# Optimization experiments

Hardware: AMD Instinct MI355X
Metric: run time of the kernel (lower is better)

Reference implementation:

```python
import jax, jax.numpy as jnp
import numpy as np
import math

N = 4096      # nodes
E = 131072    # edges (avg degree 32)
C = 128       # input channels
RATIO = 0.5   # TopKPooling default ratio
DIMS = [(128, 256), (256, 512), (512, 512), (512, 256), (256, 128)]


def setup_inputs() -> dict:
    key = jax.random.key(0)
    ks = jax.random.split(key, 16)
    inp = {}
    inp['x'] = jax.random.normal(ks[0], (N, C), jnp.float32)
    inp['edge_index'] = jax.random.randint(ks[1], (2, E), 0, N, jnp.int32)
    for i, (fi, fo) in enumerate(DIMS):
        inp[f'w{i}'] = jax.random.normal(ks[2 + i], (fi, fo), jnp.float32) / np.sqrt(fi).astype(np.float32)
        inp[f'b{i}'] = jnp.zeros((fo,), jnp.float32)
    inp['p0'] = jax.random.normal(ks[10], (256,), jnp.float32)
    inp['p1'] = jax.random.normal(ks[11], (512,), jnp.float32)
    return inp


def _gcn(x, M, w, b):
    # GCNConv: add self loops (weight 1), symmetric D^-1/2 normalization with
    # deg computed over target (col) index, aggregate messages src->dst.
    # M[r, c] = weight of edge (src=r, dst=c); dense equivalent of sparse conv.
    n = M.shape[0]
    Mc = M + jnp.eye(n, dtype=M.dtype)
    deg = Mc.sum(axis=0)
    dis = jnp.where(deg > 0, jax.lax.rsqrt(deg), 0.0)
    A = dis[:, None] * Mc * dis[None, :]          # normalized (src, dst)
    return jax.nn.relu(A.T @ (x @ w) + b)          # out[dst] = sum_src A * xW


def _augment(M):
    # augment_adj: add self loops then spspmm(A, A) -> dense (M+I) @ (M+I)
    B = M + jnp.eye(M.shape[0], dtype=M.dtype)
    return B @ B


def _pool(x, M, p):
    # TopKPooling: score = tanh(x.p / ||p||), keep top ceil(ratio*n) nodes,
    # gate kept features by score, slice adjacency to kept nodes.
    s = jnp.tanh((x @ p) / jnp.linalg.norm(p))
    k = int(math.ceil(RATIO * x.shape[0]))
    vals, perm = jax.lax.top_k(s, k)
    return x[perm] * vals[:, None], M[perm][:, perm], perm


def reference(x, edge_index, w0, b0, w1, b1, w2, b2, w3, b3, w4, b4, p0, p1):
    # dense adjacency M[src, dst] from edge list with unit edge weights
    M = jnp.zeros((N, N), jnp.float32).at[edge_index[0], edge_index[1]].add(1.0)

    # down block 0
    x = _gcn(x, M, w0, b0)
    res0, M0 = x, M
    x, M, perm0 = _pool(x, _augment(M), p0)

    # down block 1
    x = _gcn(x, M, w1, b1)
    res1, M1 = x, M
    x, M, perm1 = _pool(x, _augment(M), p1)

    # bottleneck
    x = _gcn(x, M, w2, b2)

    # up block 1: scatter into zeros, sum residual
    up = jnp.zeros_like(res1).at[perm1].set(x)
    x = _gcn(res1 + up, M1, w3, b3)

    # up block 0
    up = jnp.zeros_like(res0).at[perm0].set(x)
    x = _gcn(res0 + up, M0, w4, b4)
    return x
```

## Files before the change

kernel.cpp:

```cpp
#include <hip/hip_runtime.h>

#define NN 4096
#define EE 131072
#define NP1 2048
#define NP2 1024

typedef __attribute__((ext_vector_type(8))) __bf16 bf16x8;
typedef __attribute__((ext_vector_type(4))) float f32x4;
typedef __attribute__((ext_vector_type(8))) unsigned short ushort8;

static __device__ inline unsigned short bfbits(__bf16 b) {
  union { __bf16 x; unsigned short u; } c; c.x = b; return c.u;
}
static __device__ inline void split2(float v, unsigned short& h, unsigned short& l) {
  __bf16 hb = (__bf16)v;
  float hf = (float)hb;
  __bf16 lb = (__bf16)(v - hf);
  h = bfbits(hb); l = bfbits(lb);
}

static __device__ inline size_t pchunk(int r, int k, int NT) {
  return ((size_t)(r >> 4) * NT + (k >> 5)) * 64 + (((k >> 3) & 3) << 4) + (r & 15);
}


__global__ void hist_kernel(const int* __restrict__ src, const int* __restrict__ dst,
                            int* __restrict__ cnt_src, int* __restrict__ cnt_dst, int E) {
  int e = blockIdx.x * blockDim.x + threadIdx.x;
  if (e < E) {
    atomicAdd(&cnt_src[src[e]], 1);
    atomicAdd(&cnt_dst[dst[e]], 1);
  }
}

__global__ __launch_bounds__(1024) void scan2(const int* __restrict__ cnt_dst,
                                              const int* __restrict__ cnt_src,
                                              int* __restrict__ csc_off, int* __restrict__ csr_off,
                                              float* __restrict__ dis0, int n) {
  __shared__ int tmp[4096];
  const int* in = blockIdx.x ? cnt_src : cnt_dst;
  int* out = blockIdx.x ? csr_off : csc_off;
  int tid = threadIdx.x;
  for (int i = tid; i < n; i += 1024) {
    int v = in[i];
    tmp[i] = v;
    if (blockIdx.x == 0) dis0[i] = rsqrtf((float)v + 1.0f);
  }
  __syncthreads();
  for (int off = 1; off < n; off <<= 1) {
    int v[4];
    int c = 0;
    for (int i = tid; i < n; i += 1024) { v[c++] = (i >= off) ? tmp[i - off] : 0; }
    __syncthreads();
    c = 0;
    for (int i = tid; i < n; i += 1024) { tmp[i] += v[c++]; }
    __syncthreads();
  }
  for (int i = tid; i < n; i += 1024) out[i + 1] = tmp[i];
  if (tid == 0) out[0] = 0;
}

__global__ void scatter_kernel(const int* __restrict__ src, const int* __restrict__ dst,
                               const int* __restrict__ csc_off, const int* __restrict__ csr_off,
                               int* __restrict__ fill_dst, int* __restrict__ fill_src,
                               int* __restrict__ csc_src, int* __restrict__ csr_dst, int E) {
  int e = blockIdx.x * blockDim.x + threadIdx.x;
  if (e < E) {
    int s = src[e], d = dst[e];
    int p = atomicAdd(&fill_dst[d], 1);
    csc_src[csc_off[d] + p] = s;
    int q = atomicAdd(&fill_src[s], 1);
    csr_dst[csr_off[s] + q] = d;
  }
}

__global__ void pnorm2(const float* __restrict__ p0, const float* __restrict__ p1,
                       float* __restrict__ outv) {
  const float* p = blockIdx.x ? p1 : p0;
  int C = blockIdx.x ? 512 : 256;
  int tid = threadIdx.x;
  float acc = 0.f;
  for (int j = tid; j < C; j += 256) { float v = p[j]; acc += v * v; }
  for (int o = 32; o > 0; o >>= 1) acc += __shfl_down(acc, o);
  __shared__ float red[4];
  if ((tid & 63) == 0) red[tid >> 6] = acc;
  __syncthreads();
  if (tid == 0) outv[blockIdx.x] = sqrtf(red[0] + red[1] + red[2] + red[3]);
}


__global__ void score_key(const float* __restrict__ X, const float* __restrict__ p,
                          const float* __restrict__ pn, float* __restrict__ s,
                          unsigned long long* __restrict__ keys, int C) {
  int i = blockIdx.x;
  int tid = threadIdx.x;
  float acc = 0.f;
  for (int j = tid; j < C; j += 256) acc += X[(size_t)i * C + j] * p[j];
  for (int o = 32; o > 0; o >>= 1) acc += __shfl_down(acc, o);
  __shared__ float red[4];
  if ((tid & 63) == 0) red[tid >> 6] = acc;
  __syncthreads();
  if (tid == 0) {
    float sv = tanhf((red[0] + red[1] + red[2] + red[3]) / pn[0]);
    s[i] = sv;
    unsigned u = __float_as_uint(sv);
    unsigned m = (u & 0x80000000u) ? ~u : (u | 0x80000000u);
    keys[i] = (((unsigned long long)(~m)) << 32) | (unsigned)i;
  }
}

__global__ __launch_bounds__(256) void rank_count(const unsigned long long* __restrict__ keys,
                                                  int* __restrict__ rank) {
  __shared__ unsigned long long kk[512];
  int tid = threadIdx.x;
  int cand = blockIdx.x * 256 + tid;
  int base = blockIdx.y * 512;
  kk[tid] = keys[base + tid];
  kk[tid + 256] = keys[base + tid + 256];
  __syncthreads();
  unsigned long long kc = keys[cand];
  int c = 0;
#pragma unroll 8
  for (int t = 0; t < 512; ++t) c += (kk[t] < kc) ? 1 : 0;
  atomicAdd(&rank[cand], c);
}

__global__ void rank_place(const float* __restrict__ s, const int* __restrict__ rank, int k, int n,
                           int* __restrict__ kept, int* __restrict__ perm, float* __restrict__ vals,
                           int* __restrict__ cntk) {
  int i = blockIdx.x * blockDim.x + threadIdx.x;
  if (i < n) {
    int r = rank[i];
    int isk = (r < k) ? 1 : 0;
    if (isk) { perm[r] = i; vals[r] = s[i]; kept[i] = r; }
    else kept[i] = -1;
    if (cntk) cntk[i] = isk;
  }
}

__global__ void pool_split_p(const float* __restrict__ X, const int* __restrict__ perm,
                             const float* __restrict__ vals, unsigned short* __restrict__ h,
                             unsigned short* __restrict__ l, int C) {
  int a = blockIdx.x;
  int r = perm[a];
  float v = vals[a];
  int NT = C >> 5;
  for (int j0 = threadIdx.x * 8; j0 < C; j0 += 64 * 8) {
    ushort8 hv, lv;
#pragma unroll
    for (int e = 0; e < 8; ++e) {
      unsigned short he, le;
      split2(X[(size_t)r * C + j0 + e] * v, he, le);
      hv[e] = he; lv[e] = le;
    }
    size_t c = pchunk(a, j0, NT);
    *(ushort8*)&h[c * 8] = hv;
    *(ushort8*)&l[c * 8] = lv;
  }
}


__global__ __launch_bounds__(256) void aug_row_p(const int* __restrict__ csr_off,
                                                 const int* __restrict__ csr_dst,
                                                 const int* __restrict__ kept,
                                                 const int* __restrict__ perm,
                                                 unsigned short* __restrict__ rm) {
  __shared__ float acc[NP1];
  int ki = blockIdx.x;
  int r = perm[ki];
  for (int t = threadIdx.x; t < NP1; t += 256) acc[t] = 0.f;
  __syncthreads();
  int s = csr_off[r], e = csr_off[r + 1];
  int nm = e - s;
  int wave = threadIdx.x >> 6, lane = threadIdx.x & 63;
  for (int m = wave; m <= nm; m += 4) {
    int k = (m < nm) ? csr_dst[s + m] : r;
    int s2 = csr_off[k], e2 = csr_off[k + 1];
    int n2 = e2 - s2;
    for (int t = lane; t <= n2; t += 64) {
      int j = (t < n2) ? csr_dst[s2 + t] : k;
      int kj = kept[j];
      if (kj >= 0) atomicAdd(&acc[kj], 1.0f);
    }
  }
  __syncthreads();
  if (threadIdx.x == 0) acc[ki] += 1.0f;
  __syncthreads();
  int tid = threadIdx.x;
  ushort8 hv;
#pragma unroll
  for (int e8 = 0; e8 < 8; ++e8) hv[e8] = bfbits((__bf16)acc[tid * 8 + e8]);
  size_t dst = (((size_t)(ki >> 4)) * 64 + (tid >> 2)) * 64 + (size_t)(tid & 3) * 16 + (ki & 15);
  *(ushort8*)&rm[dst * 8] = hv;
}

__global__ void cnt_edges(const int* __restrict__ src, const int* __restrict__ dst,
                          const int* __restrict__ kept, int* __restrict__ cntk, int E) {
  int e = blockIdx.x * blockDim.x + threadIdx.x;
  if (e < E && kept[src[e]] >= 0) atomicAdd(&cntk[dst[e]], 1);
}

__global__ __launch_bounds__(256) void deg_gather(const int* __restrict__ csc_off,
                                                  const int* __restrict__ csc_src,
                                                  const int* __restrict__ cntk,
                                                  const int* __restrict__ perm,
                                                  float* __restrict__ dis) {
  int wid = threadIdx.x >> 6, lane = threadIdx.x & 63;
  int c = blockIdx.x * 4 + wid;
  int r = perm[c];
  int s = csc_off[r], e = csc_off[r + 1];
  int sum = 0;
  for (int t = s + lane; t < e; t += 64) sum += cntk[csc_src[t]];
  for (int o = 32; o > 0; o >>= 1) sum += __shfl_down(sum, o);
  if (lane == 0) dis[c] = rsqrtf((float)(sum + cntk[r] + 1));
}

__global__ __launch_bounds__(256) void t_pack(const unsigned short* __restrict__ in,
                                              unsigned short* __restrict__ outp, int n) {
  __shared__ unsigned short t[64][72];
  int r0 = blockIdx.y * 64, c0 = blockIdx.x * 64;
  int NT = n >> 5;
  for (int q = threadIdx.x; q < 512; q += 256) {
    int lt = q >> 6, l = q & 63;
    int rt = lt >> 1, kt2 = lt & 1;
    int r = rt * 16 + (l & 15), k = kt2 * 32 + (l >> 4) * 8;
    ushort8 v = *(const ushort8*)&in[pchunk(r0 + r, c0 + k, NT) * 8];
    *(ushort8*)&t[r][k] = v;
  }
  __syncthreads();
  for (int q = threadIdx.x; q < 512; q += 256) {
    int lt = q >> 6, l = q & 63;
    int jt = lt >> 1, kt2 = lt & 1;
    int j = jt * 16 + (l & 15), k = kt2 * 32 + (l >> 4) * 8;
    ushort8 v;
#pragma unroll
    for (int e = 0; e < 8; ++e) v[e] = t[k + e][j];
    *(ushort8*)&outp[pchunk(c0 + j, r0 + k, NT) * 8] = v;
  }
}

__global__ void dis_from_deg(const float* __restrict__ deg, float* __restrict__ dis, int n) {
  int i = blockIdx.x * blockDim.x + threadIdx.x;
  if (i < n) dis[i] = rsqrtf(deg[i]);
}


__global__ void split_p(const float* __restrict__ in, unsigned short* __restrict__ h,
                        unsigned short* __restrict__ l, int K) {
  int c = blockIdx.x * blockDim.x + threadIdx.x;
  int lane = c & 63, tile = c >> 6;
  int NT = K >> 5;
  int kt = tile % NT, rt = tile / NT;
  int r = rt * 16 + (lane & 15);
  int k = kt * 32 + (lane >> 4) * 8;
  const float* p = in + (size_t)r * K + k;
  ushort8 hv, lv;
#pragma unroll
  for (int e = 0; e < 8; ++e) {
    unsigned short he, le;
    split2(p[e], he, le);
    hv[e] = he; lv[e] = le;
  }
  *(ushort8*)&h[(size_t)c * 8] = hv;
  *(ushort8*)&l[(size_t)c * 8] = lv;
}

static __device__ inline void tsplit_body(const float* in, unsigned short* oh, unsigned short* ol,
                                          int R, int C, int c) {
  int lane = c & 63, tile = c >> 6;
  int NT = R >> 5;
  int kt = tile % NT, jt = tile / NT;
  int j = jt * 16 + (lane & 15);
  int k = kt * 32 + (lane >> 4) * 8;
  ushort8 hv, lv;
#pragma unroll
  for (int e = 0; e < 8; ++e) {
    unsigned short he, le;
    split2(in[(size_t)(k + e) * C + j], he, le);
    hv[e] = he; lv[e] = le;
  }
  *(ushort8*)&oh[(size_t)c * 8] = hv;
  *(ushort8*)&ol[(size_t)c * 8] = lv;
}

__global__ void tsplit_p(const float* __restrict__ in, unsigned short* __restrict__ oh,
                         unsigned short* __restrict__ ol, int R, int C) {
  int c = blockIdx.x * blockDim.x + threadIdx.x;
  tsplit_body(in, oh, ol, R, C, c);
}

__global__ void wconv_all(const float* w0, const float* w1, const float* w2,
                          const float* w3, const float* w4,
                          unsigned short* o0h, unsigned short* o0l,
                          unsigned short* o1h, unsigned short* o1l,
                          unsigned short* o2h, unsigned short* o2l,
                          unsigned short* o3h, unsigned short* o3l,
                          unsigned short* o4h, unsigned short* o4l) {
  int g = blockIdx.x * blockDim.x + threadIdx.x;
  if (g < 4096)        tsplit_body(w0, o0h, o0l, 128, 256, g);
  else if (g < 20480)  tsplit_body(w1, o1h, o1l, 256, 512, g - 4096);
  else if (g < 53248)  tsplit_body(w2, o2h, o2l, 512, 512, g - 20480);
  else if (g < 69632)  tsplit_body(w3, o3h, o3l, 512, 256, g - 53248);
  else                 tsplit_body(w4, o4h, o4l, 256, 128, g - 69632);
}

__global__ void gather_p(const unsigned short* __restrict__ in, const int* __restrict__ perm,
                         unsigned short* __restrict__ outp, int NT) {
  int c = blockIdx.x * blockDim.x + threadIdx.x;
  int lane = c & 63, tile = c >> 6;
  int kt = tile % NT, at = tile / NT;
  int a = at * 16 + (lane & 15);
  int sub = lane >> 4;
  int p = perm[a];
  size_t sc = ((size_t)(p >> 4) * NT + kt) * 64 + sub * 16 + (p & 15);
  *(ushort8*)&outp[(size_t)c * 8] = *(const ushort8*)&in[sc * 8];
}

__global__ void unpool_split_p(const float* __restrict__ res, const float* __restrict__ up,
                               const int* __restrict__ kept, unsigned short* __restrict__ h,
                               unsigned short* __restrict__ l, int C) {
  int c = blockIdx.x * blockDim.x + threadIdx.x;
  int lane = c & 63, tile = c >> 6;
  int NT = C >> 5;
  int kt = tile % NT, rt = tile / NT;
  int r = rt * 16 + (lane & 15);
  int j0 = kt * 32 + (lane >> 4) * 8;
  int kv = kept[r];
  ushort8 hv, lv;
#pragma unroll
  for (int e = 0; e < 8; ++e) {
    float v = res[(size_t)r * C + j0 + e];
    if (kv >= 0) v += up[(size_t)kv * C + j0 + e];
    unsigned short he, le;
    split2(v, he, le);
    hv[e] = he; lv[e] = le;
  }
  *(ushort8*)&h[(size_t)c * 8] = hv;
  *(ushort8*)&l[(size_t)c * 8] = lv;
}


template <int C>
__global__ __launch_bounds__(256) void spmm_gather_v(const float* __restrict__ Y,
                                                     const int* __restrict__ off,
                                                     const int* __restrict__ srcs,
                                                     const float* __restrict__ dis,
                                                     const float* __restrict__ bias,
                                                     float* __restrict__ out) {
  constexpr int VEC = C / 64;
  int w = threadIdx.x >> 6, lane = threadIdx.x & 63;
  int c = blockIdx.x * 4 + w;
  int j = lane * VEC;
  float acc[VEC];
  const float* p = Y + (size_t)c * C + j;
#pragma unroll
  for (int u = 0; u < VEC; ++u) acc[u] = p[u];
  int s = off[c], e = off[c + 1];
  for (int t = s; t < e; ++t) {
    const float* q = Y + (size_t)srcs[t] * C + j;
#pragma unroll
    for (int u = 0; u < VEC; ++u) acc[u] += q[u];
  }
  float d = dis[c];
  float* o = out + (size_t)c * C + j;
#pragma unroll
  for (int u = 0; u < VEC; ++u) o[u] = fmaxf(d * acc[u] + bias[j + u], 0.0f);
}

template <int S>
__global__ void ep3(const float* __restrict__ p, const float* __restrict__ rs,
                    const float* __restrict__ bias, float* __restrict__ outp, int M, int N) {
  int idx = blockIdx.x * blockDim.x + threadIdx.x;
  int j4 = (idx * 4) % N, i = (idx * 4) / N;
  float4 a = {0.f, 0.f, 0.f, 0.f};
#pragma unroll
  for (int s = 0; s < S; ++s) {
    float4 b = *(const float4*)(p + ((size_t)s * M + i) * N + j4);
    a.x += b.x; a.y += b.y; a.z += b.z; a.w += b.w;
  }
  float r = rs[i];
  float4 o;
  o.x = fmaxf(r * a.x + bias[j4 + 0], 0.f);
  o.y = fmaxf(r * a.y + bias[j4 + 1], 0.f);
  o.z = fmaxf(r * a.z + bias[j4 + 2], 0.f);
  o.w = fmaxf(r * a.w + bias[j4 + 3], 0.f);
  *(float4*)(outp + (size_t)i * N + j4) = o;
}

template <int S>
__global__ void ep_aug_cs(const float* __restrict__ p, float* __restrict__ B,
                          float* __restrict__ deg, int n) {
  int c = blockIdx.x * 256 + threadIdx.x;
  int r0 = blockIdx.y * 64;
  float cs = 0.f;
  for (int r = r0; r < r0 + 64; ++r) {
    float v = 0.f;
#pragma unroll
    for (int s = 0; s < S; ++s) v += p[((size_t)s * n + r) * n + c];
    if (r == c) v += 1.0f;
    B[(size_t)r * n + c] = v;
    cs += v;
  }
  atomicAdd(&deg[c], cs);
}

template <int EPI, int AL, int BL, int KK, int S>
__global__ __launch_bounds__(256) void gemm16(
    const unsigned short* __restrict__ Ah, const unsigned short* __restrict__ Al,
    const unsigned short* __restrict__ Bh, const unsigned short* __restrict__ Bl,
    int M, int N, const float* __restrict__ rs,
    float* __restrict__ C, unsigned short* __restrict__ Th, unsigned short* __restrict__ Tl) {
  static_assert(KK % 32 == 0, "K");
  constexpr int KSTEPS = KK / 32;
  const int NT = (KK * S) >> 5;
  const int gx = gridDim.x;
  int id = blockIdx.y * gx + blockIdx.x;
  int cpx = (gx * gridDim.y) >> 3;
  int sid = (id & 7) * cpx + (id >> 3);
  const int bx = sid % gx, by = sid / gx;
  const int z = (S > 1) ? blockIdx.z : 0;
  const int wid = threadIdx.x >> 6, lane = threadIdx.x & 63;
  const int i0 = by * 64 + (wid >> 1) * 32;
  const int j0 = bx * 64 + (wid & 1) * 32;
  const int lr = lane & 15, lk = lane >> 4;
  size_t aoff[2], boff[2];
#pragma unroll
  for (int t = 0; t < 2; ++t) {
    aoff[t] = ((size_t)((i0 >> 4) + t) * NT + z * (KK >> 5)) * 512 + lane * 8;
    boff[t] = ((size_t)((j0 >> 4) + t) * NT + z * (KK >> 5)) * 512 + lane * 8;
  }
  const f32x4 zf = {0.f, 0.f, 0.f, 0.f};
  f32x4 acc[2][2];
  acc[0][0] = zf; acc[0][1] = zf; acc[1][0] = zf; acc[1][1] = zf;

  bf16x8 ahf[4][2], bhf[4][2], alf[4][2], blf[4][2];
  auto loadk = [&](int kk, int b) {
    size_t o = (size_t)kk * 512;
    ahf[b][0] = *(const bf16x8*)(Ah + aoff[0] + o);
    ahf[b][1] = *(const bf16x8*)(Ah + aoff[1] + o);
    bhf[b][0] = *(const bf16x8*)(Bh + boff[0] + o);
    bhf[b][1] = *(const bf16x8*)(Bh + boff[1] + o);
    if constexpr (AL) {
      alf[b][0] = *(const bf16x8*)(Al + aoff[0] + o);
      alf[b][1] = *(const bf16x8*)(Al + aoff[1] + o);
    }
    if constexpr (BL) {
      blf[b][0] = *(const bf16x8*)(Bl + boff[0] + o);
      blf[b][1] = *(const bf16x8*)(Bl + boff[1] + o);
    }
  };
  auto domm = [&](int b) {
#pragma unroll
    for (int am = 0; am < 2; ++am)
#pragma unroll
      for (int bn = 0; bn < 2; ++bn) {
        acc[am][bn] = __builtin_amdgcn_mfma_f32_16x16x32_bf16(ahf[b][am], bhf[b][bn], acc[am][bn], 0, 0, 0);
        if constexpr (BL)
          acc[am][bn] = __builtin_amdgcn_mfma_f32_16x16x32_bf16(ahf[b][am], blf[b][bn], acc[am][bn], 0, 0, 0);
        if constexpr (AL)
          acc[am][bn] = __builtin_amdgcn_mfma_f32_16x16x32_bf16(alf[b][am], bhf[b][bn], acc[am][bn], 0, 0, 0);
      }
  };

  loadk(0, 0);
  if constexpr (KSTEPS > 1) loadk(1, 1);
  if constexpr (KSTEPS > 2) loadk(2, 2);
#pragma unroll
  for (int kk = 0; kk < KSTEPS; ++kk) {
    const int cur = kk & 3;
    if (kk + 3 < KSTEPS) loadk(kk + 3, (cur + 3) & 3);
    domm(cur);
  }

#pragma unroll
  for (int am = 0; am < 2; ++am)
#pragma unroll
    for (int bn = 0; bn < 2; ++bn) {
      int ib = i0 + 16 * am + lk * 4;
      int j = j0 + 16 * bn + lr;
      f32x4 a = acc[am][bn];
      if constexpr (S > 1) {
#pragma unroll
        for (int r = 0; r < 4; ++r) C[((size_t)z * M + ib + r) * N + j] = a[r];
      } else if constexpr (EPI == 0) {
#pragma unroll
        for (int r = 0; r < 4; ++r) C[(size_t)(ib + r) * N + j] = a[r];
      } else if constexpr (EPI == 1) {
#pragma unroll
        for (int r = 0; r < 4; ++r) C[(size_t)(ib + r) * N + j] = rs[ib + r] * a[r];
      } else {
        unsigned long long hp = 0, lp = 0;
#pragma unroll
        for (int r = 0; r < 4; ++r) {
          unsigned short hv, lv;
          split2(rs[ib + r] * a[r], hv, lv);
          hp |= ((unsigned long long)hv) << (16 * r);
          lp |= ((unsigned long long)lv) << (16 * r);
        }
        size_t c = pchunk(j, ib, M >> 5);
        *(unsigned long long*)&Th[c * 8 + (ib & 7)] = hp;
        *(unsigned long long*)&Tl[c * 8 + (ib & 7)] = lp;
      }
    }
}

template <int AL, int BL, int KK, int S>
__global__ __launch_bounds__(256) void gemm64(
    const unsigned short* __restrict__ Ah, const unsigned short* __restrict__ Al,
    const unsigned short* __restrict__ Bh, const unsigned short* __restrict__ Bl,
    int M, int N, float* __restrict__ C) {
  static_assert(KK % 32 == 0, "K");
  constexpr int KSTEPS = KK / 32;
  const int NT = (KK * S) >> 5;
  const int gx = gridDim.x;
  int id = blockIdx.y * gx + blockIdx.x;
  int cpx = (gx * gridDim.y) >> 3;
  int sid = (id & 7) * cpx + (id >> 3);
  const int bx = sid % gx, by = sid / gx;
  const int z = blockIdx.z;
  const int wid = threadIdx.x >> 6, lane = threadIdx.x & 63;
  const int i0 = by * 128 + (wid >> 1) * 64;
  const int j0 = bx * 128 + (wid & 1) * 64;
  const int lr = lane & 15, lk = lane >> 4;
  size_t aoff[4], boff[4];
#pragma unroll
  for (int t = 0; t < 4; ++t) {
    aoff[t] = ((size_t)((i0 >> 4) + t) * NT + z * (KK >> 5)) * 512 + lane * 8;
    boff[t] = ((size_t)((j0 >> 4) + t) * NT + z * (KK >> 5)) * 512 + lane * 8;
  }
  const f32x4 zf = {0.f, 0.f, 0.f, 0.f};
  f32x4 acc[4][4];
#pragma unroll
  for (int a = 0; a < 4; ++a)
#pragma unroll
    for (int b = 0; b < 4; ++b) acc[a][b] = zf;

  bf16x8 ahf[2][4], bhf[2][4], alf[2][4], blf[2][4];
  auto loadk = [&](int kk, int b) {
    size_t o = (size_t)kk * 512;
#pragma unroll
    for (int t = 0; t < 4; ++t) {
      ahf[b][t] = *(const bf16x8*)(Ah + aoff[t] + o);
      bhf[b][t] = *(const bf16x8*)(Bh + boff[t] + o);
      if constexpr (AL) alf[b][t] = *(const bf16x8*)(Al + aoff[t] + o);
      if constexpr (BL) blf[b][t] = *(const bf16x8*)(Bl + boff[t] + o);
    }
  };
  auto domm = [&](int b) {
#pragma unroll
    for (int am = 0; am < 4; ++am)
#pragma unroll
      for (int bn = 0; bn < 4; ++bn) {
        acc[am][bn] = __builtin_amdgcn_mfma_f32_16x16x32_bf16(ahf[b][am], bhf[b][bn], acc[am][bn], 0, 0, 0);
        if constexpr (BL)
          acc[am][bn] = __builtin_amdgcn_mfma_f32_16x16x32_bf16(ahf[b][am], blf[b][bn], acc[am][bn], 0, 0, 0);
        if constexpr (AL)
          acc[am][bn] = __builtin_amdgcn_mfma_f32_16x16x32_bf16(alf[b][am], bhf[b][bn], acc[am][bn], 0, 0, 0);
      }
  };

  loadk(0, 0);
#pragma unroll
  for (int kk = 0; kk < KSTEPS; ++kk) {
    const int cur = kk & 1;
    if (kk + 1 < KSTEPS) loadk(kk + 1, cur ^ 1);
    domm(cur);
  }

#pragma unroll
  for (int am = 0; am < 4; ++am)
#pragma unroll
    for (int bn = 0; bn < 4; ++bn) {
      int ib = i0 + 16 * am + lk * 4;
      int j = j0 + 16 * bn + lr;
      f32x4 a = acc[am][bn];
#pragma unroll
      for (int r = 0; r < 4; ++r) C[((size_t)z * M + ib + r) * N + j] = a[r];
    }
}


extern "C" void kernel_launch(void* const* d_in, const int* in_sizes, int n_in,
                              void* d_out, int out_size, void* d_ws, size_t ws_size,
                              hipStream_t stream) {
  (void)in_sizes; (void)n_in; (void)out_size; (void)ws_size;
  const float* x  = (const float*)d_in[0];
  const int* ei   = (const int*)d_in[1];
  const int* esrc = ei;
  const int* edst = ei + EE;
  const float* w0 = (const float*)d_in[2];
  const float* b0 = (const float*)d_in[3];
  const float* w1 = (const float*)d_in[4];
  const float* b1 = (const float*)d_in[5];
  const float* w2 = (const float*)d_in[6];
  const float* b2 = (const float*)d_in[7];
  const float* w3 = (const float*)d_in[8];
  const float* b3 = (const float*)d_in[9];
  const float* w4 = (const float*)d_in[10];
  const float* b4 = (const float*)d_in[11];
  const float* p0 = (const float*)d_in[12];
  const float* p1 = (const float*)d_in[13];
  float* out = (float*)d_out;

  char* ws = (char*)d_ws;
  size_t off = 0;
  auto alloc = [&](size_t b) { void* p = ws + off; off += (b + 255) & ~(size_t)255; return p; };

  int* csc_off = (int*)alloc(4 * (NN + 1));
  int* csr_off = (int*)alloc(4 * (NN + 1));
  int* csc_src = (int*)alloc(4 * EE);
  int* csr_dst = (int*)alloc(4 * EE);

  size_t zero_bytes = 4 * NN * 4 + 4 * NP2 + 4 * NN + 4 * NP1;
  int* cnts    = (int*)alloc(zero_bytes);
  int* cnt_dst = cnts;
  int* cnt_src = cnts + NN;
  int* fill_dst = cnts + 2 * NN;
  int* fill_src = cnts + 3 * NN;
  float* deg2 = (float*)(cnts + 4 * NN);
  int* rank0 = (int*)(deg2 + NP2);
  int* rank1 = rank0 + NN;

  int* cntk  = (int*)alloc(4 * NN);
  int* kept0 = (int*)alloc(4 * NN);
  int* perm0 = (int*)alloc(4 * NP1);
  int* kept1 = (int*)alloc(4 * NP1);
  int* perm1 = (int*)alloc(4 * NP2);
  float* dis0 = (float*)alloc(4 * NN);
  float* dis1 = (float*)alloc(4 * NP1);
  float* dis2 = (float*)alloc(4 * NP2);
  float* pnrm = (float*)alloc(8);
  float* s0   = (float*)alloc(4 * NN);
  float* vals0 = (float*)alloc(4 * NP1);
  float* s1   = (float*)alloc(4 * NP1);
  float* vals1 = (float*)alloc(4 * NP2);
  unsigned long long* keys0 = (unsigned long long*)alloc(8 * NN);
  unsigned long long* keys1 = (unsigned long long*)alloc(8 * NP1);

  const size_t MB = 1024 * 1024;
  char* regB1 = (char*)alloc(16 * MB);
  unsigned short* Gh = (unsigned short*)regB1;
  unsigned short* Hh = (unsigned short*)(regB1 + 4 * MB);
  float* B2   = (float*)regB1;
  unsigned short* B2th = (unsigned short*)(regB1 + 4 * MB);
  unsigned short* B2tl = (unsigned short*)(regB1 + 6 * MB);
  float* pscr = (float*)alloc(16 * MB);

  unsigned short* B1rm = (unsigned short*)alloc(8 * MB);
  unsigned short* B1t  = (unsigned short*)alloc(8 * MB);
  float* res0 = (float*)alloc(4 * MB);
  float* res1 = (float*)alloc(4 * MB);
  float* yreg = (float*)alloc(4 * MB);
  float* outreg = (float*)alloc(2 * MB);
  float* out2 = outreg, *out3 = outreg;
  char* ytreg = (char*)alloc(4 * MB);
  unsigned short* Y1th = (unsigned short*)ytreg;
  unsigned short* Y1tl = (unsigned short*)(ytreg + 2 * MB);
  unsigned short* Y2th = (unsigned short*)ytreg;
  unsigned short* Y2tl = (unsigned short*)(ytreg + 1 * MB);
  unsigned short* Y3th = (unsigned short*)ytreg;
  unsigned short* Y3tl = (unsigned short*)(ytreg + 1 * MB);
  char* xsreg = (char*)alloc(4 * MB);
  unsigned short* x3h = (unsigned short*)xsreg;
  unsigned short* x3l = (unsigned short*)(xsreg + 2 * MB);
  unsigned short* x4h = (unsigned short*)xsreg;
  unsigned short* x4l = (unsigned short*)(xsreg + 2 * MB);
  unsigned short* xh = (unsigned short*)alloc(1 * MB);
  unsigned short* xl = (unsigned short*)alloc(1 * MB);
  char* xsm = (char*)alloc(2 * MB);
  unsigned short* x1h = (unsigned short*)xsm;
  unsigned short* x1l = (unsigned short*)(xsm + 1 * MB);
  unsigned short* x2h = (unsigned short*)xsm;
  unsigned short* x2l = (unsigned short*)(xsm + 1 * MB);
  unsigned short* Wt0h = (unsigned short*)alloc(256 * 128 * 2);
  unsigned short* Wt0l = (unsigned short*)alloc(256 * 128 * 2);
  unsigned short* Wt1h = (unsigned short*)alloc(512 * 256 * 2);
  unsigned short* Wt1l = (unsigned short*)alloc(512 * 256 * 2);
  unsigned short* Wt2h = (unsigned short*)alloc(512 * 512 * 2);
  unsigned short* Wt2l = (unsigned short*)alloc(512 * 512 * 2);
  unsigned short* Wt3h = (unsigned short*)alloc(256 * 512 * 2);
  unsigned short* Wt3l = (unsigned short*)alloc(256 * 512 * 2);
  unsigned short* Wt4h = (unsigned short*)alloc(128 * 256 * 2);
  unsigned short* Wt4l = (unsigned short*)alloc(128 * 256 * 2);

  hipMemsetAsync(cnts, 0, zero_bytes, stream);

  hist_kernel<<<EE / 256, 256, 0, stream>>>(esrc, edst, cnt_src, cnt_dst, EE);
  scan2<<<2, 1024, 0, stream>>>(cnt_dst, cnt_src, csc_off, csr_off, dis0, NN);
  scatter_kernel<<<EE / 256, 256, 0, stream>>>(esrc, edst, csc_off, csr_off,
                                               fill_dst, fill_src, csc_src, csr_dst, EE);
  pnorm2<<<2, 256, 0, stream>>>(p0, p1, pnrm);

  wconv_all<<<288, 256, 0, stream>>>(w0, w1, w2, w3, w4, Wt0h, Wt0l, Wt1h, Wt1l,
                                     Wt2h, Wt2l, Wt3h, Wt3l, Wt4h, Wt4l);
  split_p<<<(NN * 128 / 8) / 256, 256, 0, stream>>>(x, xh, xl, 128);

  gemm16<1, 1, 1, 128, 1><<<dim3(4, 64), 256, 0, stream>>>(xh, xl, Wt0h, Wt0l,
                                                           NN, 256, dis0, yreg, nullptr, nullptr);
  spmm_gather_v<256><<<NN / 4, 256, 0, stream>>>(yreg, csc_off, csc_src, dis0, b0, res0);

  score_key<<<NN, 256, 0, stream>>>(res0, p0, pnrm + 0, s0, keys0, 256);
  rank_count<<<dim3(NN / 256, NN / 512), 256, 0, stream>>>(keys0, rank0);
  rank_place<<<NN / 256, 256, 0, stream>>>(s0, rank0, NP1, NN, kept0, perm0, vals0, cntk);
  pool_split_p<<<NP1, 64, 0, stream>>>(res0, perm0, vals0, x1h, x1l, 256);

  aug_row_p<<<NP1, 256, 0, stream>>>(csr_off, csr_dst, kept0, perm0, B1rm);
  cnt_edges<<<EE / 256, 256, 0, stream>>>(esrc, edst, kept0, cntk, EE);
  deg_gather<<<NP1 / 4, 256, 0, stream>>>(csc_off, csc_src, cntk, perm0, dis1);
  t_pack<<<dim3(32, 32), 256, 0, stream>>>(B1rm, B1t, NP1);

  gemm16<2, 1, 1, 256, 1><<<dim3(8, 32), 256, 0, stream>>>(x1h, x1l, Wt1h, Wt1l,
                                                           NP1, 512, dis1, nullptr, Y1th, Y1tl);
  gemm64<0, 1, 512, 4><<<dim3(4, 16, 4), 256, 0, stream>>>(B1t, nullptr, Y1th, Y1tl,
                                                           NP1, 512, pscr);
  ep3<4><<<(NP1 * 512) / 1024, 256, 0, stream>>>(pscr, dis1, b1, res1, NP1, 512);

  score_key<<<NP1, 256, 0, stream>>>(res1, p1, pnrm + 1, s1, keys1, 512);
  rank_count<<<dim3(NP1 / 256, NP1 / 512), 256, 0, stream>>>(keys1, rank1);
  rank_place<<<NP1 / 256, 256, 0, stream>>>(s1, rank1, NP2, NP1, kept1, perm1, vals1, nullptr);
  pool_split_p<<<NP2, 64, 0, stream>>>(res1, perm1, vals1, x2h, x2l, 512);

  gather_p<<<(NP2 * NP1 / 8) / 256, 256, 0, stream>>>(B1rm, perm1, Gh, NP1 >> 5);
  gather_p<<<(NP2 * NP1 / 8) / 256, 256, 0, stream>>>(B1t, perm1, Hh, NP1 >> 5);
  gemm64<0, 0, 512, 4><<<dim3(8, 8, 4), 256, 0, stream>>>(Gh, nullptr, Hh, nullptr,
                                                          NP2, NP2, pscr);
  ep_aug_cs<4><<<dim3(NP2 / 256, NP2 / 64), 256, 0, stream>>>(pscr, B2, deg2, NP2);
  dis_from_deg<<<NP2 / 256, 256, 0, stream>>>(deg2, dis2, NP2);
  tsplit_p<<<(NP2 * NP2 / 8) / 256, 256, 0, stream>>>(B2, B2th, B2tl, NP2, NP2);

  gemm16<2, 1, 1, 512, 1><<<dim3(8, 16), 256, 0, stream>>>(x2h, x2l, Wt2h, Wt2l,
                                                           NP2, 512, dis2, nullptr, Y2th, Y2tl);
  gemm16<0, 1, 1, 512, 2><<<dim3(8, 16, 2), 256, 0, stream>>>(B2th, B2tl, Y2th, Y2tl,
                                                              NP2, 512, nullptr, pscr, nullptr, nullptr);
  ep3<2><<<(NP2 * 512) / 1024, 256, 0, stream>>>(pscr, dis2, b2, out2, NP2, 512);

  unpool_split_p<<<(NP1 * 512 / 8) / 256, 256, 0, stream>>>(res1, out2, kept1, x3h, x3l, 512);
  gemm16<2, 1, 1, 512, 1><<<dim3(4, 32), 256, 0, stream>>>(x3h, x3l, Wt3h, Wt3l,
                                                           NP1, 256, dis1, nullptr, Y3th, Y3tl);
  gemm64<0, 1, 256, 8><<<dim3(2, 16, 8), 256, 0, stream>>>(B1t, nullptr, Y3th, Y3tl,
                                                           NP1, 256, pscr);
  ep3<8><<<(NP1 * 256) / 1024, 256, 0, stream>>>(pscr, dis1, b3, out3, NP1, 256);

  unpool_split_p<<<(NN * 256 / 8) / 256, 256, 0, stream>>>(res0, out3, kept0, x4h, x4l, 256);
  gemm16<1, 1, 1, 256, 1><<<dim3(2, 64), 256, 0, stream>>>(x4h, x4l, Wt4h, Wt4l,
                                                           NN, 128, dis0, yreg, nullptr, nullptr);
  spmm_gather_v<128><<<NN / 4, 256, 0, stream>>>(yreg, csc_off, csc_src, dis0, b4, out);
}
```

Before: 343.9 us.

## Reassociate GCN layers to aggregate before weight multiply on narrow inputs

Layers 0 and 1 now compute A·X first and then multiply by W, so the sparse or dense aggregation runs over the narrower input width (128 and 256) rather than the wider output width. Layer 0 performs a normalized sparse gather on the raw input and fuses bias plus ReLU into the GEMM epilogue. Layer 1 pre-scales the pooled features, runs the 2048x2048 adjacency GEMM at width 256 with a split-K reduction-and-split kernel, then does the weight GEMM with a fused bias/ReLU epilogue. The two gather_p launches are also merged into one. This adds kernels and extra split/transposition passes in exchange for fewer FLOPs.

```diff
diff --git a/kernel.cpp b/kernel.cpp
--- a/kernel.cpp
+++ b/kernel.cpp
@@ -136,6 +136,16 @@
     else kept[i] = -1;
     if (cntk) cntk[i] = isk;
   }
+}
+
+__global__ void pool_gather_s(const float* __restrict__ X, const int* __restrict__ perm,
+                              const float* __restrict__ vals, const float* __restrict__ dis,
+                              float* __restrict__ out, int C) {
+  int a = blockIdx.x;
+  int r = perm[a];
+  float v = vals[a] * dis[a];
+  for (int j = threadIdx.x; j < C; j += blockDim.x)
+    out[(size_t)a * C + j] = X[(size_t)r * C + j] * v;
 }
 
 __global__ void pool_split_p(const float* __restrict__ X, const int* __restrict__ perm,
@@ -304,8 +314,11 @@
   else                 tsplit_body(w4, o4h, o4l, 256, 128, g - 69632);
 }
 
-__global__ void gather_p(const unsigned short* __restrict__ in, const int* __restrict__ perm,
-                         unsigned short* __restrict__ outp, int NT) {
+__global__ void gather2_p(const unsigned short* __restrict__ in0, const unsigned short* __restrict__ in1,
+                          const int* __restrict__ perm,
+                          unsigned short* __restrict__ out0, unsigned short* __restrict__ out1, int NT) {
+  const unsigned short* in = blockIdx.y ? in1 : in0;
+  unsigned short* outp = blockIdx.y ? out1 : out0;
   int c = blockIdx.x * blockDim.x + threadIdx.x;
   int lane = c & 63, tile = c >> 6;
   int kt = tile % NT, at = tile / NT;
@@ -339,6 +352,34 @@
   *(ushort8*)&l[(size_t)c * 8] = lv;
 }
 
+
+template <int C>
+__global__ __launch_bounds__(256) void spmm_pre(const float* __restrict__ X,
+                                                const int* __restrict__ off,
+                                                const int* __restrict__ srcs,
+                                                const float* __restrict__ dis,
+                                                float* __restrict__ out) {
+  constexpr int VEC = C / 64;
+  int w = threadIdx.x >> 6, lane = threadIdx.x & 63;
+  int c = blockIdx.x * 4 + w;
+  int j = lane * VEC;
+  float dc = dis[c];
+  float acc[VEC];
+  const float* p = X + (size_t)c * C + j;
+#pragma unroll
+  for (int u = 0; u < VEC; ++u) acc[u] = dc * p[u];
+  int s = off[c], e = off[c + 1];
+  for (int t = s; t < e; ++t) {
+    int sr = srcs[t];
+    float ds = dis[sr];
+    const float* q = X + (size_t)sr * C + j;
+#pragma unroll
+    for (int u = 0; u < VEC; ++u) acc[u] += ds * q[u];
+  }
+  float* o = out + (size_t)c * C + j;
+#pragma unroll
+  for (int u = 0; u < VEC; ++u) o[u] = dc * acc[u];
+}
 
 template <int C>
 __global__ __launch_bounds__(256) void spmm_gather_v(const float* __restrict__ Y,
@@ -367,6 +408,7 @@
   for (int u = 0; u < VEC; ++u) o[u] = fmaxf(d * acc[u] + bias[j + u], 0.0f);
 }
 
+
 template <int S>
 __global__ void ep3(const float* __restrict__ p, const float* __restrict__ rs,
                     const float* __restrict__ bias, float* __restrict__ outp, int M, int N) {
@@ -385,6 +427,30 @@
   o.z = fmaxf(r * a.z + bias[j4 + 2], 0.f);
   o.w = fmaxf(r * a.w + bias[j4 + 3], 0.f);
   *(float4*)(outp + (size_t)i * N + j4) = o;
+}
+
+template <int S>
+__global__ void ep_zsplit(const float* __restrict__ p, unsigned short* __restrict__ h,
+                          unsigned short* __restrict__ l, int M, int N) {
+  int t = blockIdx.x * blockDim.x + threadIdx.x;
+  int tile = t >> 6, w = t & 63;
+  int NT = N >> 5;
+  int rt = tile / NT, kt = tile % NT;
+  int r = rt * 16 + (w & 15);
+  int k = kt * 32 + (w >> 4) * 8;
+  const float* p0 = p + (size_t)r * N + k;
+  ushort8 hv, lv;
+#pragma unroll
+  for (int e = 0; e < 8; ++e) {
+    float v = p0[e];
+#pragma unroll
+    for (int s = 1; s < S; ++s) v += p0[(size_t)s * M * N + e];
+    unsigned short he, le;
+    split2(v, he, le);
+    hv[e] = he; lv[e] = le;
+  }
+  *(ushort8*)&h[(size_t)t * 8] = hv;
+  *(ushort8*)&l[(size_t)t * 8] = lv;
 }
 
 template <int S>
@@ -408,7 +474,7 @@
 __global__ __launch_bounds__(256) void gemm16(
     const unsigned short* __restrict__ Ah, const unsigned short* __restrict__ Al,
     const unsigned short* __restrict__ Bh, const unsigned short* __restrict__ Bl,
-    int M, int N, const float* __restrict__ rs,
+    int M, int N, const float* __restrict__ rs, const float* __restrict__ bias,
     float* __restrict__ C, unsigned short* __restrict__ Th, unsigned short* __restrict__ Tl) {
   static_assert(KK % 32 == 0, "K");
   constexpr int KSTEPS = KK / 32;
@@ -488,7 +554,7 @@
       } else if constexpr (EPI == 1) {
 #pragma unroll
         for (int r = 0; r < 4; ++r) C[(size_t)(ib + r) * N + j] = rs[ib + r] * a[r];
-      } else {
+      } else if constexpr (EPI == 2) {
         unsigned long long hp = 0, lp = 0;
 #pragma unroll
         for (int r = 0; r < 4; ++r) {
@@ -500,6 +566,14 @@
         size_t c = pchunk(j, ib, M >> 5);
         *(unsigned long long*)&Th[c * 8 + (ib & 7)] = hp;
         *(unsigned long long*)&Tl[c * 8 + (ib & 7)] = lp;
+      } else if constexpr (EPI == 3) {
+#pragma unroll
+        for (int r = 0; r < 4; ++r)
+          C[(size_t)(ib + r) * N + j] = fmaxf(rs[ib + r] * a[r] + bias[j], 0.0f);
+      } else {
+#pragma unroll
+        for (int r = 0; r < 4; ++r)
+          C[(size_t)(ib + r) * N + j] = fmaxf(a[r] + bias[j], 0.0f);
       }
     }
 }
@@ -639,8 +713,8 @@
 
   const size_t MB = 1024 * 1024;
   char* regB1 = (char*)alloc(16 * MB);
-  unsigned short* Gh = (unsigned short*)regB1;
-  unsigned short* Hh = (unsigned short*)(regB1 + 4 * MB);
+  unsigned short* Gh2 = (unsigned short*)regB1;
+  unsigned short* Hh2 = (unsigned short*)(regB1 + 4 * MB);
   float* B2   = (float*)regB1;
   unsigned short* B2th = (unsigned short*)(regB1 + 4 * MB);
   unsigned short* B2tl = (unsigned short*)(regB1 + 6 * MB);
@@ -651,11 +725,11 @@
   float* res0 = (float*)alloc(4 * MB);
   float* res1 = (float*)alloc(4 * MB);
   float* yreg = (float*)alloc(4 * MB);
+  float* Gspmm = yreg;
   float* outreg = (float*)alloc(2 * MB);
+  float* x1s = outreg;
   float* out2 = outreg, *out3 = outreg;
   char* ytreg = (char*)alloc(4 * MB);
-  unsigned short* Y1th = (unsigned short*)ytreg;
-  unsigned short* Y1tl = (unsigned short*)(ytreg + 2 * MB);
   unsigned short* Y2th = (unsigned short*)ytreg;
   unsigned short* Y2tl = (unsigned short*)(ytreg + 1 * MB);
   unsigned short* Y3th = (unsigned short*)ytreg;
@@ -668,8 +742,10 @@
   unsigned short* xh = (unsigned short*)alloc(1 * MB);
   unsigned short* xl = (unsigned short*)alloc(1 * MB);
   char* xsm = (char*)alloc(2 * MB);
-  unsigned short* x1h = (unsigned short*)xsm;
-  unsigned short* x1l = (unsigned short*)(xsm + 1 * MB);
+  unsigned short* x1th = (unsigned short*)xsm;
+  unsigned short* x1tl = (unsigned short*)(xsm + 1 * MB);
+  unsigned short* Zh = (unsigned short*)xsm;
+  unsigned short* Zl = (unsigned short*)(xsm + 1 * MB);
   unsigned short* x2h = (unsigned short*)xsm;
   unsigned short* x2l = (unsigned short*)(xsm + 1 * MB);
   unsigned short* Wt0h = (unsigned short*)alloc(256 * 128 * 2);
@@ -690,59 +766,58 @@
   scatter_kernel<<<EE / 256, 256, 0, stream>>>(esrc, edst, csc_off, csr_off,
                                                fill_dst, fill_src, csc_src, csr_dst, EE);
   pnorm2<<<2, 256, 0, stream>>>(p0, p1, pnrm);
-
   wconv_all<<<288, 256, 0, stream>>>(w0, w1, w2, w3, w4, Wt0h, Wt0l, Wt1h, Wt1l,
                                      Wt2h, Wt2l, Wt3h, Wt3l, Wt4h, Wt4l);
-  split_p<<<(NN * 128 / 8) / 256, 256, 0, stream>>>(x, xh, xl, 128);
-
-  gemm16<1, 1, 1, 128, 1><<<dim3(4, 64), 256, 0, stream>>>(xh, xl, Wt0h, Wt0l,
-                                                           NN, 256, dis0, yreg, nullptr, nullptr);
-  spmm_gather_v<256><<<NN / 4, 256, 0, stream>>>(yreg, csc_off, csc_src, dis0, b0, res0);
+
+  spmm_pre<128><<<NN / 4, 256, 0, stream>>>(x, csc_off, csc_src, dis0, Gspmm);
+  split_p<<<(NN * 128 / 8) / 256, 256, 0, stream>>>(Gspmm, xh, xl, 128);
+  gemm16<4, 1, 1, 128, 1><<<dim3(4, 64), 256, 0, stream>>>(xh, xl, Wt0h, Wt0l,
+                                                           NN, 256, nullptr, b0, res0, nullptr, nullptr);
 
   score_key<<<NN, 256, 0, stream>>>(res0, p0, pnrm + 0, s0, keys0, 256);
   rank_count<<<dim3(NN / 256, NN / 512), 256, 0, stream>>>(keys0, rank0);
   rank_place<<<NN / 256, 256, 0, stream>>>(s0, rank0, NP1, NN, kept0, perm0, vals0, cntk);
-  pool_split_p<<<NP1, 64, 0, stream>>>(res0, perm0, vals0, x1h, x1l, 256);
 
   aug_row_p<<<NP1, 256, 0, stream>>>(csr_off, csr_dst, kept0, perm0, B1rm);
   cnt_edges<<<EE / 256, 256, 0, stream>>>(esrc, edst, kept0, cntk, EE);
   deg_gather<<<NP1 / 4, 256, 0, stream>>>(csc_off, csc_src, cntk, perm0, dis1);
   t_pack<<<dim3(32, 32), 256, 0, stream>>>(B1rm, B1t, NP1);
 
-  gemm16<2, 1, 1, 256, 1><<<dim3(8, 32), 256, 0, stream>>>(x1h, x1l, Wt1h, Wt1l,
-                                                           NP1, 512, dis1, nullptr, Y1th, Y1tl);
-  gemm64<0, 1, 512, 4><<<dim3(4, 16, 4), 256, 0, stream>>>(B1t, nullptr, Y1th, Y1tl,
-                                                           NP1, 512, pscr);
-  ep3<4><<<(NP1 * 512) / 1024, 256, 0, stream>>>(pscr, dis1, b1, res1, NP1, 512);
+  pool_gather_s<<<NP1, 256, 0, stream>>>(res0, perm0, vals0, dis1, x1s, 256);
+  tsplit_p<<<(NP1 * 256 / 8) / 256, 256, 0, stream>>>(x1s, x1th, x1tl, NP1, 256);
+  gemm16<0, 0, 1, 1024, 2><<<dim3(4, 32, 2), 256, 0, stream>>>(B1t, nullptr, x1th, x1tl,
+                                                               NP1, 256, nullptr, nullptr, pscr, nullptr, nullptr);
+  ep_zsplit<2><<<(NP1 * 256 / 8) / 256, 256, 0, stream>>>(pscr, Zh, Zl, NP1, 256);
+  gemm16<3, 1, 1, 256, 1><<<dim3(8, 32), 256, 0, stream>>>(Zh, Zl, Wt1h, Wt1l,
+                                                           NP1, 512, dis1, b1, res1, nullptr, nullptr);
 
   score_key<<<NP1, 256, 0, stream>>>(res1, p1, pnrm + 1, s1, keys1, 512);
   rank_count<<<dim3(NP1 / 256, NP1 / 512), 256, 0, stream>>>(keys1, rank1);
   rank_place<<<NP1 / 256, 256, 0, stream>>>(s1, rank1, NP2, NP1, kept1, perm1, vals1, nullptr);
   pool_split_p<<<NP2, 64, 0, stream>>>(res1, perm1, vals1, x2h, x2l, 512);
 
-  gather_p<<<(NP2 * NP1 / 8) / 256, 256, 0, stream>>>(B1rm, perm1, Gh, NP1 >> 5);
-  gather_p<<<(NP2 * NP1 / 8) / 256, 256, 0, stream>>>(B1t, perm1, Hh, NP1 >> 5);
-  gemm64<0, 0, 512, 4><<<dim3(8, 8, 4), 256, 0, stream>>>(Gh, nullptr, Hh, nullptr,
+  gather2_p<<<dim3((NP2 * NP1 / 8) / 256, 2), 256, 0, stream>>>(B1rm, B1t, perm1, Gh2, Hh2, NP1 >> 5);
+  gemm64<0, 0, 512, 4><<<dim3(8, 8, 4), 256, 0, stream>>>(Gh2, nullptr, Hh2, nullptr,
                                                           NP2, NP2, pscr);
   ep_aug_cs<4><<<dim3(NP2 / 256, NP2 / 64), 256, 0, stream>>>(pscr, B2, deg2, NP2);
   dis_from_deg<<<NP2 / 256, 256, 0, stream>>>(deg2, dis2, NP2);
   tsplit_p<<<(NP2 * NP2 / 8) / 256, 256, 0, stream>>>(B2, B2th, B2tl, NP2, NP2);
 
   gemm16<2, 1, 1, 512, 1><<<dim3(8, 16), 256, 0, stream>>>(x2h, x2l, Wt2h, Wt2l,
-                                                           NP2, 512, dis2, nullptr, Y2th, Y2tl);
+                                                           NP2, 512, dis2, nullptr, nullptr, Y2th, Y2tl);
   gemm16<0, 1, 1, 512, 2><<<dim3(8, 16, 2), 256, 0, stream>>>(B2th, B2tl, Y2th, Y2tl,
-                                                              NP2, 512, nullptr, pscr, nullptr, nullptr);
+                                                              NP2, 512, nullptr, nullptr, pscr, nullptr, nullptr);
   ep3<2><<<(NP2 * 512) / 1024, 256, 0, stream>>>(pscr, dis2, b2, out2, NP2, 512);
 
   unpool_split_p<<<(NP1 * 512 / 8) / 256, 256, 0, stream>>>(res1, out2, kept1, x3h, x3l, 512);
   gemm16<2, 1, 1, 512, 1><<<dim3(4, 32), 256, 0, stream>>>(x3h, x3l, Wt3h, Wt3l,
-                                                           NP1, 256, dis1, nullptr, Y3th, Y3tl);
+                                                           NP1, 256, dis1, nullptr, nullptr, Y3th, Y3tl);
   gemm64<0, 1, 256, 8><<<dim3(2, 16, 8), 256, 0, stream>>>(B1t, nullptr, Y3th, Y3tl,
                                                            NP1, 256, pscr);
   ep3<8><<<(NP1 * 256) / 1024, 256, 0, stream>>>(pscr, dis1, b3, out3, NP1, 256);
 
   unpool_split_p<<<(NN * 256 / 8) / 256, 256, 0, stream>>>(res0, out3, kept0, x4h, x4l, 256);
   gemm16<1, 1, 1, 256, 1><<<dim3(2, 64), 256, 0, stream>>>(x4h, x4l, Wt4h, Wt4l,
-                                                           NN, 128, dis0, yreg, nullptr, nullptr);
+                                                           NN, 128, dis0, nullptr, yreg, nullptr, nullptr);
   spmm_gather_v<128><<<NN / 4, 256, 0, stream>>>(yreg, csc_off, csc_src, dis0, b4, out);
 }
```

Result: no change. 339.8 us (-1.2%).
